# Performance work log

Measured on AMD Instinct MI355X. Metric: run time of the kernel, lower is better.

The kernel has to match this reference:

```python
import jax, jax.numpy as jnp
import numpy as np

B, N, D = 128, 1024, 512  # batch, num_neurons, d_model


def setup_inputs() -> dict:
    key = jax.random.key(0)
    kx, kw, kb = jax.random.split(key, 3)
    x = jax.random.normal(kx, (B, N, 1), dtype=jnp.float32)
    # Stacked weights/biases of the num_neurons Linear(1, d_model) layers.
    # torch Linear(1, d_model): weight [d_model, 1], bias [d_model]; stacked -> [N, D].
    W = jax.random.normal(kw, (N, D), dtype=jnp.float32) * (1.0)  # kaiming-uniform-ish scale irrelevant for correctness
    b = jax.random.normal(kb, (N, D), dtype=jnp.float32) * 0.01
    return {"x": x, "W": W, "b": b}


def reference(x, W, b):
    # out[b,i,d] = x[b,i,0] * W[i,d] + b[i,d]
    # Fused equivalent of: stack([Linear_i(x[:, i, :]) for i in range(N)], dim=1)
    return x * W[None, :, :] + b[None, :, :]
```

## Files before the change

### kernel.cpp

```cpp
#include <hip/hip_runtime.h>
#include <hip/hip_bf16.h>


constexpr int kB   = 128;
constexpr int kN   = 1024;
constexpr int kD4  = 512 / 4;
constexpr int kBG  = 8;
constexpr int kRowStride4 = kN * kD4;

typedef float v4f __attribute__((ext_vector_type(4)));

__global__ __launch_bounds__(256) void bcast_fma_kernel(
    const float* __restrict__ x,
    const v4f*   __restrict__ W,
    const v4f*   __restrict__ bias,
    v4f*         __restrict__ out)
{
    const int wave = threadIdx.x >> 6;
    const int lane = threadIdx.x & 63;
    const int w    = (blockIdx.x << 2) + wave;
    const int i    = w & (kN - 1);
    const int bg   = w >> 10;

    const int wb = i * kD4;
    const v4f w0 = W[wb + lane];
    const v4f w1 = W[wb + lane + 64];
    const v4f b0 = bias[wb + lane];
    const v4f b1 = bias[wb + lane + 64];

    float xv[kBG];
#pragma unroll
    for (int g = 0; g < kBG; ++g)
        xv[g] = x[(bg * kBG + g) * kN + i];

    const long ob = (long)(bg * kBG) * kRowStride4 + (long)i * kD4 + lane;

#pragma unroll
    for (int g = 0; g < kBG; ++g) {
        const float xg = xv[g];
        v4f o0, o1;
        o0.x = fmaf(xg, w0.x, b0.x);
        o0.y = fmaf(xg, w0.y, b0.y);
        o0.z = fmaf(xg, w0.z, b0.z);
        o0.w = fmaf(xg, w0.w, b0.w);
        o1.x = fmaf(xg, w1.x, b1.x);
        o1.y = fmaf(xg, w1.y, b1.y);
        o1.z = fmaf(xg, w1.z, b1.z);
        o1.w = fmaf(xg, w1.w, b1.w);
        __builtin_nontemporal_store(o0, &out[ob + (long)g * kRowStride4]);
        __builtin_nontemporal_store(o1, &out[ob + (long)g * kRowStride4 + 64]);
    }
}

extern "C" void kernel_launch(void* const* d_in, const int* in_sizes, int n_in,
                              void* d_out, int out_size, void* d_ws, size_t ws_size,
                              hipStream_t stream) {
    const float* x    = (const float*)d_in[0];
    const v4f*   W    = (const v4f*)d_in[1];
    const v4f*   bias = (const v4f*)d_in[2];
    v4f*         out  = (v4f*)d_out;

    constexpr int kWaves = kN * (kB / kBG);
    constexpr int kGrid  = kWaves / 4;
    bcast_fma_kernel<<<kGrid, 256, 0, stream>>>(x, W, bias, out);
}
```

Before: 269.5 us.

## Remap waves to contiguous 64-row output slabs per batch with shuffled x

Each wave now handles one batch element and 64 consecutive neurons, reading W and bias per row inside the loop, loading x once per lane and broadcasting it with a wave shuffle. Before, each wave kept one neuron's W/b in registers and wrote 8 rows strided across batches. The new mapping writes one contiguous output region per wave, aiming at better write locality and fewer scattered stores. The cost is that W and b are reloaded for every batch (up to 128x reuse now relies on L2/MALL caching), which raises read traffic.

```diff
diff --git a/kernel.cpp b/kernel.cpp
--- a/kernel.cpp
+++ b/kernel.cpp
@@ -1,12 +1,9 @@
 #include <hip/hip_runtime.h>
-#include <hip/hip_bf16.h>
 
 
-constexpr int kB   = 128;
-constexpr int kN   = 1024;
-constexpr int kD4  = 512 / 4;
-constexpr int kBG  = 8;
-constexpr int kRowStride4 = kN * kD4;
+constexpr int kN    = 1024;
+constexpr int kD4   = 512 / 4;
+constexpr int kRows = 64;
 
 typedef float v4f __attribute__((ext_vector_type(4)));
 
@@ -19,36 +16,33 @@
     const int wave = threadIdx.x >> 6;
     const int lane = threadIdx.x & 63;
     const int w    = (blockIdx.x << 2) + wave;
-    const int i    = w & (kN - 1);
-    const int bg   = w >> 10;
+    const int b    = w >> 4;
+    const int i0   = (w & 15) * kRows;
 
-    const int wb = i * kD4;
-    const v4f w0 = W[wb + lane];
-    const v4f w1 = W[wb + lane + 64];
-    const v4f b0 = bias[wb + lane];
-    const v4f b1 = bias[wb + lane + 64];
+    const float xl = x[b * kN + i0 + lane];
 
-    float xv[kBG];
-#pragma unroll
-    for (int g = 0; g < kBG; ++g)
-        xv[g] = x[(bg * kBG + g) * kN + i];
+    const int  wb = i0 * kD4 + lane;
+    const long ob = (long)b * (kN * kD4) + wb;
 
-    const long ob = (long)(bg * kBG) * kRowStride4 + (long)i * kD4 + lane;
-
-#pragma unroll
-    for (int g = 0; g < kBG; ++g) {
-        const float xg = xv[g];
+#pragma unroll 4
+    for (int r = 0; r < kRows; ++r) {
+        const float xr = __shfl(xl, r, 64);
+        const int   o  = r * kD4;
+        const v4f w0 = W[wb + o];
+        const v4f w1 = W[wb + o + 64];
+        const v4f c0 = bias[wb + o];
+        const v4f c1 = bias[wb + o + 64];
         v4f o0, o1;
-        o0.x = fmaf(xg, w0.x, b0.x);
-        o0.y = fmaf(xg, w0.y, b0.y);
-        o0.z = fmaf(xg, w0.z, b0.z);
-        o0.w = fmaf(xg, w0.w, b0.w);
-        o1.x = fmaf(xg, w1.x, b1.x);
-        o1.y = fmaf(xg, w1.y, b1.y);
-        o1.z = fmaf(xg, w1.z, b1.z);
-        o1.w = fmaf(xg, w1.w, b1.w);
-        __builtin_nontemporal_store(o0, &out[ob + (long)g * kRowStride4]);
-        __builtin_nontemporal_store(o1, &out[ob + (long)g * kRowStride4 + 64]);
+        o0.x = fmaf(xr, w0.x, c0.x);
+        o0.y = fmaf(xr, w0.y, c0.y);
+        o0.z = fmaf(xr, w0.z, c0.z);
+        o0.w = fmaf(xr, w0.w, c0.w);
+        o1.x = fmaf(xr, w1.x, c1.x);
+        o1.y = fmaf(xr, w1.y, c1.y);
+        o1.z = fmaf(xr, w1.z, c1.z);
+        o1.w = fmaf(xr, w1.w, c1.w);
+        __builtin_nontemporal_store(o0, &out[ob + o]);
+        __builtin_nontemporal_store(o1, &out[ob + o + 64]);
     }
 }
 
@@ -60,7 +54,7 @@
     const v4f*   bias = (const v4f*)d_in[2];
     v4f*         out  = (v4f*)d_out;
 
-    constexpr int kWaves = kN * (kB / kBG);
+    constexpr int kWaves = 128 * (kN / kRows);
     constexpr int kGrid  = kWaves / 4;
     bcast_fma_kernel<<<kGrid, 256, 0, stream>>>(x, W, bias, out);
 }
```

Result: slower. 313.8 us (+16.4%).
